# Performance work log

Measured on AMD Instinct MI355X. Metric: run time of the kernel, lower is better.

Reference implementation:

```python
import jax, jax.numpy as jnp
import numpy as np

BITS = 8
STEP = 2.0 ** (-5)
QMIN = -2.0 ** (BITS - 1)
QMAX = 2.0 ** (BITS - 1) - 1


def _q(x):
    # DFXP fixed-point fake-quantize: clamp(round(x/step), qmin, qmax)*step
    return jnp.clip(jnp.round(x / STEP), QMIN, QMAX) * STEP


@jax.custom_vjp
def fq(x):
    # ForwardQuantizer: quantize in fwd, straight-through grad
    return _q(x)

def _fq_fwd(x):
    return _q(x), None

def _fq_bwd(_, g):
    return (g,)

fq.defvjp(_fq_fwd, _fq_bwd)


def gq(x):
    # BackwardQuantizer: identity in forward (grad quantized only in bwd pass)
    return x


def setup_inputs() -> dict:
    key = jax.random.key(0)
    ks = jax.random.split(key, 5)
    B, I, H = 2048, 1024, 1024
    return {
        "X": jax.random.normal(ks[0], (B, I), dtype=jnp.float32),
        "h": jax.random.normal(ks[1], (B, H), dtype=jnp.float32),
        "c": jax.random.normal(ks[2], (B, H), dtype=jnp.float32),
        "weight": jax.random.normal(ks[3], (4 * H, I + H), dtype=jnp.float32) * (H ** -0.5),
        "bias": jax.random.normal(ks[4], (4 * H,), dtype=jnp.float32) * (H ** -0.5),
    }


def reference(X, h, c, weight, bias):
    # concat + input/weight/bias fake-quant
    Xh = fq(jnp.concatenate([X, h], axis=1))          # [B, I+H]
    Wq = fq(weight)                                    # [4H, I+H]
    bq = fq(bias)                                      # [4H]
    y = gq(Xh @ Wq.T + bq)                             # [B, 4H]
    i, f, g, o = jnp.split(y, 4, axis=1)
    i = fq(gq(jax.nn.sigmoid(i)))
    f = fq(gq(jax.nn.sigmoid(f)))
    g = fq(gq(jnp.tanh(g)))
    o = fq(gq(jax.nn.sigmoid(o)))
    cq = fq(c)
    c_new = gq(cq * f) + gq(i * g)
    cell_tanh = fq(gq(jnp.tanh(c_new)))
    h_new = gq(cell_tanh * o)
    return (h_new, c_new)
```

## Files before the change

kernel.cpp:

```cpp
#include <hip/hip_runtime.h>
#include <stdint.h>

#define B_DIM 2048
#define K_DIM 2048
#define N_PACK 4096

typedef int v4i __attribute__((ext_vector_type(4)));

__device__ __forceinline__ float fqf(float x) {
    float q = rintf(x * 32.0f);
    q = fminf(fmaxf(q, -128.0f), 127.0f);
    return q * 0.03125f;
}
__device__ __forceinline__ int q8i(float x) {
    float q = rintf(x * 32.0f);
    q = fminf(fmaxf(q, -128.0f), 127.0f);
    return (int)q;
}
__device__ __forceinline__ float fsigm(float x) {
    return __fdividef(1.0f, 1.0f + __expf(-x));
}
__device__ __forceinline__ float ftanh(float x) {
    return __fdividef(2.0f, 1.0f + __expf(-2.0f * x)) - 1.0f;
}

__global__ __launch_bounds__(256) void quant_pack(
    const float* __restrict__ X, const float* __restrict__ hI,
    const float* __restrict__ W, const float* __restrict__ bias,
    int8_t* __restrict__ Xhq, int8_t* __restrict__ Wq, float* __restrict__ bqp)
{
    const int bid = blockIdx.x;
    const int t = threadIdx.x;
    if (bid < B_DIM) {
        const int m = bid;
        const int k0 = t * 8;
        const float* src = (k0 < 1024) ? (X + (size_t)m * 1024 + k0)
                                       : (hI + (size_t)m * 1024 + (k0 - 1024));
        float4 v0 = *(const float4*)src;
        float4 v1 = *(const float4*)(src + 4);
        union { int8_t c[8]; int64_t ll; } u;
        u.c[0] = (int8_t)q8i(v0.x); u.c[1] = (int8_t)q8i(v0.y);
        u.c[2] = (int8_t)q8i(v0.z); u.c[3] = (int8_t)q8i(v0.w);
        u.c[4] = (int8_t)q8i(v1.x); u.c[5] = (int8_t)q8i(v1.y);
        u.c[6] = (int8_t)q8i(v1.z); u.c[7] = (int8_t)q8i(v1.w);
        *(int64_t*)(Xhq + (size_t)m * K_DIM + k0) = u.ll;
    } else if (bid < B_DIM + N_PACK) {
        const int r = bid - B_DIM;
        const int gate = r >> 10, j = r & 1023;
        const int p = (j << 2) | gate;
        const int k0 = t * 8;
        const float* src = W + (size_t)r * K_DIM + k0;
        float4 v0 = *(const float4*)src;
        float4 v1 = *(const float4*)(src + 4);
        union { int8_t c[8]; int64_t ll; } u;
        u.c[0] = (int8_t)q8i(v0.x); u.c[1] = (int8_t)q8i(v0.y);
        u.c[2] = (int8_t)q8i(v0.z); u.c[3] = (int8_t)q8i(v0.w);
        u.c[4] = (int8_t)q8i(v1.x); u.c[5] = (int8_t)q8i(v1.y);
        u.c[6] = (int8_t)q8i(v1.z); u.c[7] = (int8_t)q8i(v1.w);
        *(int64_t*)(Wq + (size_t)p * K_DIM + k0) = u.ll;
    } else {
        for (int idx = t; idx < N_PACK; idx += 256) {
            const int gate = idx >> 10, j = idx & 1023;
            bqp[(j << 2) | gate] = fqf(bias[idx]);
        }
    }
}

__global__ __launch_bounds__(512) void lstm_gemm(
    const int8_t* __restrict__ Xhq, const int8_t* __restrict__ Wq,
    const float* __restrict__ bqp, const float* __restrict__ cin,
    float* __restrict__ hout, float* __restrict__ cout_)
{
    __shared__ __align__(16) char raw[65536];
    const int t = threadIdx.x;
    const int l = t & 63;
    const int wave = t >> 6;
    const int wm = wave >> 2;
    const int wn = wave & 3;

    const int b = blockIdx.x;
    const int xcd = b & 7;
    const int slot = b >> 3;
    const int mt = ((xcd & 1) << 3) + (slot & 7);
    const int nt = ((xcd >> 1) << 3) + (slot >> 3);
    const int m0 = mt * 128;
    const int n0 = nt * 128;

    v4i acc[4][2];
    #pragma unroll
    for (int i = 0; i < 4; ++i)
        #pragma unroll
        for (int j = 0; j < 2; ++j)
            acc[i][j] = (v4i)0;

    const int srow = t >> 3;
    const int schunk = (t & 7) ^ (srow & 7);
    const int8_t* gA = Xhq + (size_t)(m0 + srow) * K_DIM + schunk * 16;
    const int8_t* gB = Wq  + (size_t)(n0 + srow) * K_DIM + schunk * 16;

    const int rrow = l & 15;
    const int lx = l & 7;

#define STAGE(p, kt) do { \
    char* Ad_ = raw + (p) * 32768; \
    char* Bd_ = raw + (p) * 32768 + 16384; \
    _Pragma("unroll") \
    for (int i_ = 0; i_ < 2; ++i_) { \
        __builtin_amdgcn_global_load_lds( \
            (const __attribute__((address_space(1))) uint32_t*)(gA + (size_t)(i_ * 64) * K_DIM + (kt) * 128), \
            (__attribute__((address_space(3))) uint32_t*)(Ad_ + i_ * 8192 + t * 16), 16, 0, 0); \
        __builtin_amdgcn_global_load_lds( \
            (const __attribute__((address_space(1))) uint32_t*)(gB + (size_t)(i_ * 64) * K_DIM + (kt) * 128), \
            (__attribute__((address_space(3))) uint32_t*)(Bd_ + i_ * 8192 + t * 16), 16, 0, 0); \
    } \
} while (0)

    STAGE(0, 0);

    for (int kt = 0; kt < 16; ++kt) {
        const int p = kt & 1;
        if (kt < 15) {
            STAGE(p ^ 1, kt + 1);
            asm volatile("s_waitcnt vmcnt(4)" ::: "memory");
        } else {
            asm volatile("s_waitcnt vmcnt(0)" ::: "memory");
        }
        asm volatile("s_barrier" ::: "memory");

        const char* As = raw + p * 32768;
        const char* Bs = raw + p * 32768 + 16384;
        v4i a[2][4], b2[2][2];
        #pragma unroll
        for (int kk = 0; kk < 2; ++kk) {
            const int c = kk * 4 + (l >> 4);
            const int sl = (c ^ lx) * 16;
            #pragma unroll
            for (int mf = 0; mf < 4; ++mf) {
                const int r = wm * 64 + mf * 16 + rrow;
                a[kk][mf] = *(const v4i*)(As + r * 128 + sl);
            }
            #pragma unroll
            for (int nf = 0; nf < 2; ++nf) {
                const int r = wn * 32 + nf * 16 + rrow;
                b2[kk][nf] = *(const v4i*)(Bs + r * 128 + sl);
            }
        }
        #pragma unroll
        for (int kk = 0; kk < 2; ++kk)
            #pragma unroll
            for (int mf = 0; mf < 4; ++mf)
                #pragma unroll
                for (int nf = 0; nf < 2; ++nf)
                    acc[mf][nf] = __builtin_amdgcn_mfma_i32_16x16x64_i8(a[kk][mf], b2[kk][nf], acc[mf][nf], 0, 0, 0);
        asm volatile("s_waitcnt lgkmcnt(0)" ::: "memory");
        asm volatile("s_barrier" ::: "memory");
    }

    float (*Cs)[132] = (float(*)[132])raw;
    const float sc = 0.0009765625f;
    for (int half = 0; half < 2; ++half) {
        __syncthreads();
        if (wm == half) {
            #pragma unroll
            for (int mf = 0; mf < 4; ++mf) {
                const int rb = mf * 16 + ((l >> 4) << 2);
                #pragma unroll
                for (int nf = 0; nf < 2; ++nf) {
                    const int col = wn * 32 + nf * 16 + (l & 15);
                    #pragma unroll
                    for (int rr = 0; rr < 4; ++rr)
                        Cs[rb + rr][col] = (float)acc[mf][nf][rr] * sc;
                }
            }
        }
        __syncthreads();
        #pragma unroll
        for (int it = 0; it < 4; ++it) {
            const int idx = it * 512 + t;
            const int row = idx >> 5;
            const int jl = idx & 31;
            float4 y = *(const float4*)&Cs[row][jl << 2];
            float4 bb = *(const float4*)&bqp[n0 + (jl << 2)];
            const int m = m0 + half * 64 + row;
            const int j = (n0 >> 2) + jl;
            const float ig = fqf(fsigm(y.x + bb.x));
            const float fg = fqf(fsigm(y.y + bb.y));
            const float gg = fqf(ftanh(y.z + bb.z));
            const float og = fqf(fsigm(y.w + bb.w));
            const float cq = fqf(cin[(size_t)m * 1024 + j]);
            const float cn = cq * fg + ig * gg;
            const float hn = fqf(ftanh(cn)) * og;
            hout[(size_t)m * 1024 + j] = hn;
            cout_[(size_t)m * 1024 + j] = cn;
        }
    }
}

extern "C" void kernel_launch(void* const* d_in, const int* in_sizes, int n_in,
                              void* d_out, int out_size, void* d_ws, size_t ws_size,
                              hipStream_t stream) {
    const float* X    = (const float*)d_in[0];
    const float* h    = (const float*)d_in[1];
    const float* c    = (const float*)d_in[2];
    const float* W    = (const float*)d_in[3];
    const float* bias = (const float*)d_in[4];

    float* out   = (float*)d_out;
    float* h_out = out;
    float* c_out = out + (size_t)B_DIM * 1024;

    char* ws = (char*)d_ws;
    int8_t* Xhq = (int8_t*)ws;
    int8_t* Wq  = (int8_t*)(ws + (size_t)4 * 1024 * 1024);
    float*  bqp = (float*)(ws + (size_t)12 * 1024 * 1024);

    quant_pack<<<B_DIM + N_PACK + 1, 256, 0, stream>>>(X, h, W, bias, Xhq, Wq, bqp);

    lstm_gemm<<<512, 512, 0, stream>>>(Xhq, Wq, bqp, c, h_out, c_out);
}
```

Measured before the change: 41.08 us.

## Enlarge GEMM tile to 256x128 with triple-buffered LDS and interleaved loads

Doubles the M tile per block to 256 rows, halving the grid to 256 blocks. It replaces double buffering with a three-stage LDS ring of 144KB and spreads the next-next stage's global-to-LDS loads across four sub-steps interleaved with MFMA work, using s_setprio around MFMAs. This aims to raise reuse of B fragments and hide memory latency better. The cost is fewer blocks than CUs (256 on a 256-CU part, one per CU), more accumulator registers, and more barriers per K step.

```diff
diff --git a/kernel.cpp b/kernel.cpp
--- a/kernel.cpp
+++ b/kernel.cpp
@@ -71,7 +71,7 @@
     const float* __restrict__ bqp, const float* __restrict__ cin,
     float* __restrict__ hout, float* __restrict__ cout_)
 {
-    __shared__ __align__(16) char raw[65536];
+    __shared__ __align__(16) char raw[147456];
     const int t = threadIdx.x;
     const int l = t & 63;
     const int wave = t >> 6;
@@ -81,14 +81,14 @@
     const int b = blockIdx.x;
     const int xcd = b & 7;
     const int slot = b >> 3;
-    const int mt = ((xcd & 1) << 3) + (slot & 7);
-    const int nt = ((xcd >> 1) << 3) + (slot >> 3);
-    const int m0 = mt * 128;
+    const int mt = ((xcd & 1) << 2) + (slot & 3);
+    const int nt = ((xcd >> 1) << 3) + (slot >> 2);
+    const int m0 = mt * 256;
     const int n0 = nt * 128;
 
-    v4i acc[4][2];
+    v4i acc[8][2];
     #pragma unroll
-    for (int i = 0; i < 4; ++i)
+    for (int i = 0; i < 8; ++i)
         #pragma unroll
         for (int j = 0; j < 2; ++j)
             acc[i][j] = (v4i)0;
@@ -98,78 +98,90 @@
     const int8_t* gA = Xhq + (size_t)(m0 + srow) * K_DIM + schunk * 16;
     const int8_t* gB = Wq  + (size_t)(n0 + srow) * K_DIM + schunk * 16;
 
+#define LDA(sb, kt, i) __builtin_amdgcn_global_load_lds( \
+    (const __attribute__((address_space(1))) uint32_t*)(gA + (size_t)((i) * 64) * K_DIM + (size_t)(kt) * 128), \
+    (__attribute__((address_space(3))) uint32_t*)(raw + (sb) + (i) * 8192 + t * 16), 16, 0, 0)
+#define LDB(sb, kt, i) __builtin_amdgcn_global_load_lds( \
+    (const __attribute__((address_space(1))) uint32_t*)(gB + (size_t)((i) * 64) * K_DIM + (size_t)(kt) * 128), \
+    (__attribute__((address_space(3))) uint32_t*)(raw + (sb) + 32768 + (i) * 8192 + t * 16), 16, 0, 0)
+
+    LDA(0, 0, 0); LDA(0, 0, 1); LDA(0, 0, 2); LDA(0, 0, 3);
+    LDB(0, 0, 0); LDB(0, 0, 1);
+    LDA(49152, 1, 0); LDA(49152, 1, 1); LDA(49152, 1, 2); LDA(49152, 1, 3);
+    LDB(49152, 1, 0); LDB(49152, 1, 1);
+    asm volatile("s_waitcnt vmcnt(6)" ::: "memory");
+    __builtin_amdgcn_s_barrier();
+
     const int rrow = l & 15;
     const int lx = l & 7;
-
-#define STAGE(p, kt) do { \
-    char* Ad_ = raw + (p) * 32768; \
-    char* Bd_ = raw + (p) * 32768 + 16384; \
-    _Pragma("unroll") \
-    for (int i_ = 0; i_ < 2; ++i_) { \
-        __builtin_amdgcn_global_load_lds( \
-            (const __attribute__((address_space(1))) uint32_t*)(gA + (size_t)(i_ * 64) * K_DIM + (kt) * 128), \
-            (__attribute__((address_space(3))) uint32_t*)(Ad_ + i_ * 8192 + t * 16), 16, 0, 0); \
-        __builtin_amdgcn_global_load_lds( \
-            (const __attribute__((address_space(1))) uint32_t*)(gB + (size_t)(i_ * 64) * K_DIM + (kt) * 128), \
-            (__attribute__((address_space(3))) uint32_t*)(Bd_ + i_ * 8192 + t * 16), 16, 0, 0); \
-    } \
-} while (0)
-
-    STAGE(0, 0);
-
+    const int ccol = l >> 4;
+
+    int sA = 0;
+    int sN = 2 * 49152;
     for (int kt = 0; kt < 16; ++kt) {
-        const int p = kt & 1;
-        if (kt < 15) {
-            STAGE(p ^ 1, kt + 1);
-            asm volatile("s_waitcnt vmcnt(4)" ::: "memory");
-        } else {
-            asm volatile("s_waitcnt vmcnt(0)" ::: "memory");
-        }
-        asm volatile("s_barrier" ::: "memory");
-
-        const char* As = raw + p * 32768;
-        const char* Bs = raw + p * 32768 + 16384;
-        v4i a[2][4], b2[2][2];
+        const char* As = raw + sA;
+        const char* Bs = As + 32768;
+        const bool st = kt < 14;
+        v4i bfr[2][2];
         #pragma unroll
-        for (int kk = 0; kk < 2; ++kk) {
-            const int c = kk * 4 + (l >> 4);
-            const int sl = (c ^ lx) * 16;
+        for (int q = 0; q < 4; ++q) {
+            v4i afr[2][2];
             #pragma unroll
-            for (int mf = 0; mf < 4; ++mf) {
-                const int r = wm * 64 + mf * 16 + rrow;
-                a[kk][mf] = *(const v4i*)(As + r * 128 + sl);
+            for (int kk = 0; kk < 2; ++kk) {
+                const int sl = ((kk * 4 + ccol) ^ lx) * 16;
+                if (q == 0) {
+                    #pragma unroll
+                    for (int nf = 0; nf < 2; ++nf)
+                        bfr[kk][nf] = *(const v4i*)(Bs + (wn * 32 + nf * 16 + rrow) * 128 + sl);
+                }
+                #pragma unroll
+                for (int mi = 0; mi < 2; ++mi)
+                    afr[kk][mi] = *(const v4i*)(As + (wm * 128 + (q * 2 + mi) * 16 + rrow) * 128 + sl);
             }
+            if (st) {
+                if (q == 0)      { LDA(sN, kt + 2, 0); LDA(sN, kt + 2, 1); }
+                else if (q == 1) { LDA(sN, kt + 2, 2); LDA(sN, kt + 2, 3); }
+                else if (q == 2) { LDB(sN, kt + 2, 0); }
+                else             { LDB(sN, kt + 2, 1); }
+            }
+            __builtin_amdgcn_s_barrier();
+            __builtin_amdgcn_s_setprio(1);
             #pragma unroll
-            for (int nf = 0; nf < 2; ++nf) {
-                const int r = wn * 32 + nf * 16 + rrow;
-                b2[kk][nf] = *(const v4i*)(Bs + r * 128 + sl);
-            }
-        }
-        #pragma unroll
-        for (int kk = 0; kk < 2; ++kk)
-            #pragma unroll
-            for (int mf = 0; mf < 4; ++mf)
+            for (int kk = 0; kk < 2; ++kk)
                 #pragma unroll
-                for (int nf = 0; nf < 2; ++nf)
-                    acc[mf][nf] = __builtin_amdgcn_mfma_i32_16x16x64_i8(a[kk][mf], b2[kk][nf], acc[mf][nf], 0, 0, 0);
-        asm volatile("s_waitcnt lgkmcnt(0)" ::: "memory");
-        asm volatile("s_barrier" ::: "memory");
+                for (int mi = 0; mi < 2; ++mi)
+                    #pragma unroll
+                    for (int nf = 0; nf < 2; ++nf)
+                        acc[q * 2 + mi][nf] = __builtin_amdgcn_mfma_i32_16x16x64_i8(
+                            afr[kk][mi], bfr[kk][nf], acc[q * 2 + mi][nf], 0, 0, 0);
+            __builtin_amdgcn_s_setprio(0);
+            if (q < 3) __builtin_amdgcn_s_barrier();
+        }
+        if (kt < 14)       asm volatile("s_waitcnt vmcnt(6)" ::: "memory");
+        else if (kt == 14) asm volatile("s_waitcnt vmcnt(0)" ::: "memory");
+        if (kt < 15) __builtin_amdgcn_s_barrier();
+        sA += 49152; if (sA == 147456) sA = 0;
+        sN += 49152; if (sN == 147456) sN = 0;
     }
+
+#undef LDA
+#undef LDB
 
     float (*Cs)[132] = (float(*)[132])raw;
     const float sc = 0.0009765625f;
-    for (int half = 0; half < 2; ++half) {
+    for (int qr = 0; qr < 4; ++qr) {
         __syncthreads();
-        if (wm == half) {
+        if (wm == (qr >> 1)) {
+            const int mfb = (qr & 1) * 4;
             #pragma unroll
-            for (int mf = 0; mf < 4; ++mf) {
-                const int rb = mf * 16 + ((l >> 4) << 2);
+            for (int mf2 = 0; mf2 < 4; ++mf2) {
+                const int rb = mf2 * 16 + ((l >> 4) << 2);
                 #pragma unroll
                 for (int nf = 0; nf < 2; ++nf) {
                     const int col = wn * 32 + nf * 16 + (l & 15);
                     #pragma unroll
                     for (int rr = 0; rr < 4; ++rr)
-                        Cs[rb + rr][col] = (float)acc[mf][nf][rr] * sc;
+                        Cs[rb + rr][col] = (float)acc[mfb + mf2][nf][rr] * sc;
                 }
             }
         }
@@ -180,13 +192,13 @@
             const int row = idx >> 5;
             const int jl = idx & 31;
             float4 y = *(const float4*)&Cs[row][jl << 2];
-            float4 bb = *(const float4*)&bqp[n0 + (jl << 2)];
-            const int m = m0 + half * 64 + row;
+            float4 bv = *(const float4*)&bqp[n0 + (jl << 2)];
+            const int m = m0 + qr * 64 + row;
             const int j = (n0 >> 2) + jl;
-            const float ig = fqf(fsigm(y.x + bb.x));
-            const float fg = fqf(fsigm(y.y + bb.y));
-            const float gg = fqf(ftanh(y.z + bb.z));
-            const float og = fqf(fsigm(y.w + bb.w));
+            const float ig = fqf(fsigm(y.x + bv.x));
+            const float fg = fqf(fsigm(y.y + bv.y));
+            const float gg = fqf(ftanh(y.z + bv.z));
+            const float og = fqf(fsigm(y.w + bv.w));
             const float cq = fqf(cin[(size_t)m * 1024 + j]);
             const float cn = cq * fg + ig * gg;
             const float hn = fqf(ftanh(cn)) * og;
@@ -216,5 +228,5 @@
 
     quant_pack<<<B_DIM + N_PACK + 1, 256, 0, stream>>>(X, h, W, bias, Xhq, Wq, bqp);
 
-    lstm_gemm<<<512, 512, 0, stream>>>(Xhq, Wq, bqp, c, h_out, c_out);
-}
+    lstm_gemm<<<256, 512, 0, stream>>>(Xhq, Wq, bqp, c, h_out, c_out);
+}
```

Measured after the change: 58.56 us. 1.43x slower.

## Pre-swizzle weights into MFMA fragment layout and load B directly to registers

Applied to the files above, without the earlier changes.

The quant kernel now packs the int8 weights into a fragment-ordered layout via an LDS transpose, so the GEMM can load B operands straight from global memory into registers without staging them in LDS. The GEMM tile widens to 128x256 with a K-step of 256, halving the grid to 256 blocks, and only A is staged through double-buffered LDS. The goal is to cut LDS traffic and barriers per MFMA and to raise reuse of A. The cost is more register pressure from the larger accumulators and the prefetched B buffers, and fewer blocks than CUs.

```diff
diff --git a/kernel.cpp b/kernel.cpp
--- a/kernel.cpp
+++ b/kernel.cpp
@@ -27,8 +27,9 @@
 __global__ __launch_bounds__(256) void quant_pack(
     const float* __restrict__ X, const float* __restrict__ hI,
     const float* __restrict__ W, const float* __restrict__ bias,
-    int8_t* __restrict__ Xhq, int8_t* __restrict__ Wq, float* __restrict__ bqp)
+    int8_t* __restrict__ Xhq, int8_t* __restrict__ Wq2, float* __restrict__ bqp)
 {
+    __shared__ __align__(16) char lds[16 * 2064];
     const int bid = blockIdx.x;
     const int t = threadIdx.x;
     if (bid < B_DIM) {
@@ -44,20 +45,28 @@
         u.c[4] = (int8_t)q8i(v1.x); u.c[5] = (int8_t)q8i(v1.y);
         u.c[6] = (int8_t)q8i(v1.z); u.c[7] = (int8_t)q8i(v1.w);
         *(int64_t*)(Xhq + (size_t)m * K_DIM + k0) = u.ll;
-    } else if (bid < B_DIM + N_PACK) {
-        const int r = bid - B_DIM;
-        const int gate = r >> 10, j = r & 1023;
-        const int p = (j << 2) | gate;
-        const int k0 = t * 8;
-        const float* src = W + (size_t)r * K_DIM + k0;
-        float4 v0 = *(const float4*)src;
-        float4 v1 = *(const float4*)(src + 4);
-        union { int8_t c[8]; int64_t ll; } u;
-        u.c[0] = (int8_t)q8i(v0.x); u.c[1] = (int8_t)q8i(v0.y);
-        u.c[2] = (int8_t)q8i(v0.z); u.c[3] = (int8_t)q8i(v0.w);
-        u.c[4] = (int8_t)q8i(v1.x); u.c[5] = (int8_t)q8i(v1.y);
-        u.c[6] = (int8_t)q8i(v1.z); u.c[7] = (int8_t)q8i(v1.w);
-        *(int64_t*)(Wq + (size_t)p * K_DIM + k0) = u.ll;
+    } else if (bid < B_DIM + 256) {
+        const int c0 = bid - B_DIM;
+        for (int pi = 0; pi < 16; ++pi) {
+            const int r = (pi & 3) * 1024 + c0 * 4 + (pi >> 2);
+            const float* src = W + (size_t)r * K_DIM + t * 8;
+            float4 v0 = *(const float4*)src;
+            float4 v1 = *(const float4*)(src + 4);
+            union { int8_t c[8]; int64_t ll; } u;
+            u.c[0] = (int8_t)q8i(v0.x); u.c[1] = (int8_t)q8i(v0.y);
+            u.c[2] = (int8_t)q8i(v0.z); u.c[3] = (int8_t)q8i(v0.w);
+            u.c[4] = (int8_t)q8i(v1.x); u.c[5] = (int8_t)q8i(v1.y);
+            u.c[6] = (int8_t)q8i(v1.z); u.c[7] = (int8_t)q8i(v1.w);
+            *(int64_t*)(lds + pi * 2064 + t * 8) = u.ll;
+        }
+        __syncthreads();
+        const int w = t >> 6, l = t & 63;
+        #pragma unroll
+        for (int rd = 0; rd < 8; ++rd) {
+            const int c = rd * 4 + w;
+            v4i val = *(const v4i*)(lds + (l & 15) * 2064 + c * 64 + (l >> 4) * 16);
+            *(v4i*)(Wq2 + ((size_t)c0 << 15) + c * 1024 + l * 16) = val;
+        }
     } else {
         for (int idx = t; idx < N_PACK; idx += 256) {
             const int gate = idx >> 10, j = idx & 1023;
@@ -67,7 +76,7 @@
 }
 
 __global__ __launch_bounds__(512) void lstm_gemm(
-    const int8_t* __restrict__ Xhq, const int8_t* __restrict__ Wq,
+    const int8_t* __restrict__ Xhq, const int8_t* __restrict__ Wq2,
     const float* __restrict__ bqp, const float* __restrict__ cin,
     float* __restrict__ hout, float* __restrict__ cout_)
 {
@@ -82,91 +91,115 @@
     const int xcd = b & 7;
     const int slot = b >> 3;
     const int mt = ((xcd & 1) << 3) + (slot & 7);
-    const int nt = ((xcd >> 1) << 3) + (slot >> 3);
+    const int nt = ((xcd >> 1) << 2) + (slot >> 3);
     const int m0 = mt * 128;
-    const int n0 = nt * 128;
-
-    v4i acc[4][2];
+    const int n0 = nt * 256;
+
+    v4i acc[4][4];
     #pragma unroll
     for (int i = 0; i < 4; ++i)
         #pragma unroll
-        for (int j = 0; j < 2; ++j)
+        for (int j = 0; j < 4; ++j)
             acc[i][j] = (v4i)0;
 
-    const int srow = t >> 3;
-    const int schunk = (t & 7) ^ (srow & 7);
+    const int srow = t >> 4;
+    const int schunk = (t & 15) ^ (srow & 7);
     const int8_t* gA = Xhq + (size_t)(m0 + srow) * K_DIM + schunk * 16;
-    const int8_t* gB = Wq  + (size_t)(n0 + srow) * K_DIM + schunk * 16;
+
+#define STAGE_A(kt) do { \
+    char* Ad_ = raw + (((kt) & 1) ? 32768 : 0); \
+    _Pragma("unroll") \
+    for (int i_ = 0; i_ < 4; ++i_) { \
+        __builtin_amdgcn_global_load_lds( \
+            (const __attribute__((address_space(1))) uint32_t*)(gA + (size_t)(i_) * 65536 + (size_t)(kt) * 256), \
+            (__attribute__((address_space(3))) uint32_t*)(Ad_ + i_ * 8192 + t * 16), 16, 0, 0); \
+    } \
+} while (0)
+
+    const int8_t* gBw = Wq2 + (((size_t)(n0 >> 4) + wn * 4) << 15) + (size_t)l * 16;
+#define LOADB(dst, h) do { \
+    _Pragma("unroll") \
+    for (int nf_ = 0; nf_ < 4; ++nf_) \
+        _Pragma("unroll") \
+        for (int kk_ = 0; kk_ < 2; ++kk_) \
+            dst[kk_][nf_] = *(const v4i*)(gBw + ((size_t)nf_ << 15) + (size_t)((h) * 2 + kk_) * 1024); \
+} while (0)
+
+    v4i b0[2][4], b1[2][4];
+    STAGE_A(0);
+    LOADB(b0, 0);
+    LOADB(b1, 1);
 
     const int rrow = l & 15;
     const int lx = l & 7;
-
-#define STAGE(p, kt) do { \
-    char* Ad_ = raw + (p) * 32768; \
-    char* Bd_ = raw + (p) * 32768 + 16384; \
-    _Pragma("unroll") \
-    for (int i_ = 0; i_ < 2; ++i_) { \
-        __builtin_amdgcn_global_load_lds( \
-            (const __attribute__((address_space(1))) uint32_t*)(gA + (size_t)(i_ * 64) * K_DIM + (kt) * 128), \
-            (__attribute__((address_space(3))) uint32_t*)(Ad_ + i_ * 8192 + t * 16), 16, 0, 0); \
-        __builtin_amdgcn_global_load_lds( \
-            (const __attribute__((address_space(1))) uint32_t*)(gB + (size_t)(i_ * 64) * K_DIM + (kt) * 128), \
-            (__attribute__((address_space(3))) uint32_t*)(Bd_ + i_ * 8192 + t * 16), 16, 0, 0); \
-    } \
-} while (0)
-
-    STAGE(0, 0);
-
-    for (int kt = 0; kt < 16; ++kt) {
-        const int p = kt & 1;
-        if (kt < 15) {
-            STAGE(p ^ 1, kt + 1);
-            asm volatile("s_waitcnt vmcnt(4)" ::: "memory");
-        } else {
-            asm volatile("s_waitcnt vmcnt(0)" ::: "memory");
-        }
+    const int g4 = l >> 4;
+
+    for (int kt = 0; kt < 8; ++kt) {
+        const char* As = raw + ((kt & 1) ? 32768 : 0);
+        if (kt < 7) STAGE_A(kt + 1);
+        if (kt < 7) asm volatile("s_waitcnt vmcnt(12)" ::: "memory");
+        else        asm volatile("s_waitcnt vmcnt(8)" ::: "memory");
         asm volatile("s_barrier" ::: "memory");
 
-        const char* As = raw + p * 32768;
-        const char* Bs = raw + p * 32768 + 16384;
-        v4i a[2][4], b2[2][2];
-        #pragma unroll
-        for (int kk = 0; kk < 2; ++kk) {
-            const int c = kk * 4 + (l >> 4);
-            const int sl = (c ^ lx) * 16;
-            #pragma unroll
-            for (int mf = 0; mf < 4; ++mf) {
-                const int r = wm * 64 + mf * 16 + rrow;
-                a[kk][mf] = *(const v4i*)(As + r * 128 + sl);
+        {
+            v4i a[2][4];
+            #pragma unroll
+            for (int kk = 0; kk < 2; ++kk) {
+                const int sl = ((kk * 4 + g4) ^ lx) * 16;
+                #pragma unroll
+                for (int mf = 0; mf < 4; ++mf)
+                    a[kk][mf] = *(const v4i*)(As + (size_t)(wm * 64 + mf * 16 + rrow) * 256 + sl);
             }
             #pragma unroll
-            for (int nf = 0; nf < 2; ++nf) {
-                const int r = wn * 32 + nf * 16 + rrow;
-                b2[kk][nf] = *(const v4i*)(Bs + r * 128 + sl);
+            for (int kk = 0; kk < 2; ++kk)
+                #pragma unroll
+                for (int mf = 0; mf < 4; ++mf)
+                    #pragma unroll
+                    for (int nf = 0; nf < 4; ++nf)
+                        acc[mf][nf] = __builtin_amdgcn_mfma_i32_16x16x64_i8(
+                            a[kk][mf], b0[kk][nf], acc[mf][nf], 0, 0, 0);
+        }
+        if (kt < 7) LOADB(b0, 2 * kt + 2);
+        {
+            v4i a[2][4];
+            #pragma unroll
+            for (int kk = 0; kk < 2; ++kk) {
+                const int sl = (((2 + kk) * 4 + g4) ^ lx) * 16;
+                #pragma unroll
+                for (int mf = 0; mf < 4; ++mf)
+                    a[kk][mf] = *(const v4i*)(As + (size_t)(wm * 64 + mf * 16 + rrow) * 256 + sl);
             }
-        }
-        #pragma unroll
-        for (int kk = 0; kk < 2; ++kk)
-            #pragma unroll
-            for (int mf = 0; mf < 4; ++mf)
-                #pragma unroll
-                for (int nf = 0; nf < 2; ++nf)
-                    acc[mf][nf] = __builtin_amdgcn_mfma_i32_16x16x64_i8(a[kk][mf], b2[kk][nf], acc[mf][nf], 0, 0, 0);
+            if (kt < 7) asm volatile("s_waitcnt vmcnt(8)" ::: "memory");
+            else        asm volatile("s_waitcnt vmcnt(0)" ::: "memory");
+            #pragma unroll
+            for (int kk = 0; kk < 2; ++kk)
+                #pragma unroll
+                for (int mf = 0; mf < 4; ++mf)
+                    #pragma unroll
+                    for (int nf = 0; nf < 4; ++nf)
+                        acc[mf][nf] = __builtin_amdgcn_mfma_i32_16x16x64_i8(
+                            a[kk][mf], b1[kk][nf], acc[mf][nf], 0, 0, 0);
+        }
+        if (kt < 7) LOADB(b1, 2 * kt + 3);
         asm volatile("s_waitcnt lgkmcnt(0)" ::: "memory");
         asm volatile("s_barrier" ::: "memory");
     }
 
-    float (*Cs)[132] = (float(*)[132])raw;
+#undef STAGE_A
+#undef LOADB
+
+    float (*Cs)[264] = (float(*)[264])raw;
     const float sc = 0.0009765625f;
-    for (int half = 0; half < 2; ++half) {
+    for (int q = 0; q < 4; ++q) {
         __syncthreads();
-        if (wm == half) {
-            #pragma unroll
-            for (int mf = 0; mf < 4; ++mf) {
-                const int rb = mf * 16 + ((l >> 4) << 2);
-                #pragma unroll
-                for (int nf = 0; nf < 2; ++nf) {
-                    const int col = wn * 32 + nf * 16 + (l & 15);
+        if (wm == (q >> 1)) {
+            #pragma unroll
+            for (int mf2 = 0; mf2 < 2; ++mf2) {
+                const int mf = (q & 1) * 2 + mf2;
+                const int rb = mf2 * 16 + ((l >> 4) << 2);
+                #pragma unroll
+                for (int nf = 0; nf < 4; ++nf) {
+                    const int col = wn * 64 + nf * 16 + (l & 15);
                     #pragma unroll
                     for (int rr = 0; rr < 4; ++rr)
                         Cs[rb + rr][col] = (float)acc[mf][nf][rr] * sc;
@@ -177,16 +210,16 @@
         #pragma unroll
         for (int it = 0; it < 4; ++it) {
             const int idx = it * 512 + t;
-            const int row = idx >> 5;
-            const int jl = idx & 31;
+            const int row = idx >> 6;
+            const int jl = idx & 63;
             float4 y = *(const float4*)&Cs[row][jl << 2];
-            float4 bb = *(const float4*)&bqp[n0 + (jl << 2)];
-            const int m = m0 + half * 64 + row;
+            float4 bv = *(const float4*)&bqp[n0 + (jl << 2)];
+            const int m = m0 + q * 32 + row;
             const int j = (n0 >> 2) + jl;
-            const float ig = fqf(fsigm(y.x + bb.x));
-            const float fg = fqf(fsigm(y.y + bb.y));
-            const float gg = fqf(ftanh(y.z + bb.z));
-            const float og = fqf(fsigm(y.w + bb.w));
+            const float ig = fqf(fsigm(y.x + bv.x));
+            const float fg = fqf(fsigm(y.y + bv.y));
+            const float gg = fqf(ftanh(y.z + bv.z));
+            const float og = fqf(fsigm(y.w + bv.w));
             const float cq = fqf(cin[(size_t)m * 1024 + j]);
             const float cn = cq * fg + ig * gg;
             const float hn = fqf(ftanh(cn)) * og;
@@ -211,10 +244,10 @@
 
     char* ws = (char*)d_ws;
     int8_t* Xhq = (int8_t*)ws;
-    int8_t* Wq  = (int8_t*)(ws + (size_t)4 * 1024 * 1024);
+    int8_t* Wq2 = (int8_t*)(ws + (size_t)4 * 1024 * 1024);
     float*  bqp = (float*)(ws + (size_t)12 * 1024 * 1024);
 
-    quant_pack<<<B_DIM + N_PACK + 1, 256, 0, stream>>>(X, h, W, bias, Xhq, Wq, bqp);
-
-    lstm_gemm<<<512, 512, 0, stream>>>(Xhq, Wq, bqp, c, h_out, c_out);
-}
+    quant_pack<<<B_DIM + 256 + 1, 256, 0, stream>>>(X, h, W, bias, Xhq, Wq2, bqp);
+
+    lstm_gemm<<<256, 512, 0, stream>>>(Xhq, Wq2, bqp, c, h_out, c_out);
+}
```

After: 63.51 us. +54.6%, slower.

## Deepen GEMM pipeline to four stages with smaller K tiles and one barrier

Applied to the files above, without the earlier changes.

Restructures the int8 GEMM main loop from a double-buffered 128-wide K tile into a four-slot ring of 64-wide K tiles, prefetching three stages ahead with one barrier per iteration instead of two. The LDS layout and swizzle change so two rows pack into each 128-byte line, and s_setprio wraps the MFMA block. Launch bounds now request 4 waves per SIMD. The aim is better overlap of global-to-LDS loads with MFMA work and less barrier overhead, at the cost of more iterations, more complex indexing, and a possible bank-conflict change.

```diff
diff --git a/kernel.cpp b/kernel.cpp
--- a/kernel.cpp
+++ b/kernel.cpp
@@ -66,7 +66,7 @@
     }
 }
 
-__global__ __launch_bounds__(512) void lstm_gemm(
+__global__ __launch_bounds__(512, 4) void lstm_gemm(
     const int8_t* __restrict__ Xhq, const int8_t* __restrict__ Wq,
     const float* __restrict__ bqp, const float* __restrict__ cin,
     float* __restrict__ hout, float* __restrict__ cout_)
@@ -93,68 +93,67 @@
         for (int j = 0; j < 2; ++j)
             acc[i][j] = (v4i)0;
 
-    const int srow = t >> 3;
-    const int schunk = (t & 7) ^ (srow & 7);
-    const int8_t* gA = Xhq + (size_t)(m0 + srow) * K_DIM + schunk * 16;
-    const int8_t* gB = Wq  + (size_t)(n0 + srow) * K_DIM + schunk * 16;
+    const int rp_s = t >> 3;
+    const int u_s = (t & 7) ^ (rp_s & 7);
+    const int grow = 2 * rp_s + (u_s >> 2);
+    const int gcol = (u_s & 3) * 16;
+    const int8_t* gA = Xhq + (size_t)(m0 + grow) * K_DIM + gcol;
+    const int8_t* gB = Wq  + (size_t)(n0 + grow) * K_DIM + gcol;
+
+#define STAGE(p, kt) do { \
+    __builtin_amdgcn_global_load_lds( \
+        (const __attribute__((address_space(1))) uint32_t*)(gA + (size_t)(kt) * 64), \
+        (__attribute__((address_space(3))) uint32_t*)(raw + (p) * 16384 + t * 16), 16, 0, 0); \
+    __builtin_amdgcn_global_load_lds( \
+        (const __attribute__((address_space(1))) uint32_t*)(gB + (size_t)(kt) * 64), \
+        (__attribute__((address_space(3))) uint32_t*)(raw + (p) * 16384 + 8192 + t * 16), 16, 0, 0); \
+} while (0)
+
+    STAGE(0, 0); STAGE(1, 1); STAGE(2, 2);
 
     const int rrow = l & 15;
-    const int lx = l & 7;
-
-#define STAGE(p, kt) do { \
-    char* Ad_ = raw + (p) * 32768; \
-    char* Bd_ = raw + (p) * 32768 + 16384; \
+    const int rp = rrow >> 1;
+    const int g4 = l >> 4;
+    const int soff = (((g4 | ((rrow & 1) << 2)) ^ (rp & 7)) << 4);
+
+#define COMPUTE(kt) do { \
+    const char* As_ = raw + ((kt) & 3) * 16384; \
+    const char* Bs_ = As_ + 8192; \
+    v4i a_[4], b_[2]; \
     _Pragma("unroll") \
-    for (int i_ = 0; i_ < 2; ++i_) { \
-        __builtin_amdgcn_global_load_lds( \
-            (const __attribute__((address_space(1))) uint32_t*)(gA + (size_t)(i_ * 64) * K_DIM + (kt) * 128), \
-            (__attribute__((address_space(3))) uint32_t*)(Ad_ + i_ * 8192 + t * 16), 16, 0, 0); \
-        __builtin_amdgcn_global_load_lds( \
-            (const __attribute__((address_space(1))) uint32_t*)(gB + (size_t)(i_ * 64) * K_DIM + (kt) * 128), \
-            (__attribute__((address_space(3))) uint32_t*)(Bd_ + i_ * 8192 + t * 16), 16, 0, 0); \
-    } \
+    for (int mf = 0; mf < 4; ++mf) \
+        a_[mf] = *(const v4i*)(As_ + (wm * 32 + mf * 8 + rp) * 128 + soff); \
+    _Pragma("unroll") \
+    for (int nf = 0; nf < 2; ++nf) \
+        b_[nf] = *(const v4i*)(Bs_ + (wn * 16 + nf * 8 + rp) * 128 + soff); \
+    __builtin_amdgcn_s_setprio(1); \
+    _Pragma("unroll") \
+    for (int mf = 0; mf < 4; ++mf) \
+        _Pragma("unroll") \
+        for (int nf = 0; nf < 2; ++nf) \
+            acc[mf][nf] = __builtin_amdgcn_mfma_i32_16x16x64_i8( \
+                a_[mf], b_[nf], acc[mf][nf], 0, 0, 0); \
+    __builtin_amdgcn_s_setprio(0); \
 } while (0)
 
-    STAGE(0, 0);
-
-    for (int kt = 0; kt < 16; ++kt) {
-        const int p = kt & 1;
-        if (kt < 15) {
-            STAGE(p ^ 1, kt + 1);
-            asm volatile("s_waitcnt vmcnt(4)" ::: "memory");
-        } else {
-            asm volatile("s_waitcnt vmcnt(0)" ::: "memory");
-        }
+    for (int kt = 0; kt < 29; ++kt) {
+        asm volatile("s_waitcnt vmcnt(4)" ::: "memory");
         asm volatile("s_barrier" ::: "memory");
-
-        const char* As = raw + p * 32768;
-        const char* Bs = raw + p * 32768 + 16384;
-        v4i a[2][4], b2[2][2];
-        #pragma unroll
-        for (int kk = 0; kk < 2; ++kk) {
-            const int c = kk * 4 + (l >> 4);
-            const int sl = (c ^ lx) * 16;
-            #pragma unroll
-            for (int mf = 0; mf < 4; ++mf) {
-                const int r = wm * 64 + mf * 16 + rrow;
-                a[kk][mf] = *(const v4i*)(As + r * 128 + sl);
-            }
-            #pragma unroll
-            for (int nf = 0; nf < 2; ++nf) {
-                const int r = wn * 32 + nf * 16 + rrow;
-                b2[kk][nf] = *(const v4i*)(Bs + r * 128 + sl);
-            }
-        }
-        #pragma unroll
-        for (int kk = 0; kk < 2; ++kk)
-            #pragma unroll
-            for (int mf = 0; mf < 4; ++mf)
-                #pragma unroll
-                for (int nf = 0; nf < 2; ++nf)
-                    acc[mf][nf] = __builtin_amdgcn_mfma_i32_16x16x64_i8(a[kk][mf], b2[kk][nf], acc[mf][nf], 0, 0, 0);
-        asm volatile("s_waitcnt lgkmcnt(0)" ::: "memory");
-        asm volatile("s_barrier" ::: "memory");
+        STAGE((kt + 3) & 3, kt + 3);
+        COMPUTE(kt);
     }
+    asm volatile("s_waitcnt vmcnt(4)" ::: "memory");
+    asm volatile("s_barrier" ::: "memory");
+    COMPUTE(29);
+    asm volatile("s_waitcnt vmcnt(2)" ::: "memory");
+    asm volatile("s_barrier" ::: "memory");
+    COMPUTE(30);
+    asm volatile("s_waitcnt vmcnt(0)" ::: "memory");
+    asm volatile("s_barrier" ::: "memory");
+    COMPUTE(31);
+
+#undef STAGE
+#undef COMPUTE
 
     float (*Cs)[132] = (float(*)[132])raw;
     const float sc = 0.0009765625f;
```

Result: slower. 42.15 us (+2.6%).
